# Kernel tuning notes

Measured on AMD Instinct MI355X. Metric: run time of the kernel, lower is better.

The kernel has to match this reference:

```python
import jax, jax.numpy as jnp
import numpy as np

NEG_SLOPE = 0.2  # PyG GATConv default LeakyReLU slope
EPS = 1e-16      # PyG softmax denominator epsilon


def _gat_layer(x, src, dst, W, a_src, a_dst, b, H, C):
    """One PyG-style GATConv layer (eval mode, add_self_loops already applied).
    x: [N, F_in], W: [F_in, H*C], a_src/a_dst: [H, C], b: [H*C]."""
    N = x.shape[0]
    h = (x @ W).reshape(N, H, C)                       # [N,H,C]
    alpha_src = jnp.sum(h * a_src, axis=-1)            # [N,H]
    alpha_dst = jnp.sum(h * a_dst, axis=-1)            # [N,H]
    e = jax.nn.leaky_relu(alpha_src[src] + alpha_dst[dst], NEG_SLOPE)  # [E,H]
    m = jax.ops.segment_max(e, dst, num_segments=N)    # [N,H] segment-softmax max
    p = jnp.exp(e - m[dst])                            # [E,H]
    s = jax.ops.segment_sum(p, dst, num_segments=N)    # [N,H]
    attn = p / (s[dst] + EPS)                          # [E,H]
    out = jax.ops.segment_sum(attn[:, :, None] * h[src], dst, num_segments=N)  # [N,H,C]
    return out.reshape(N, H * C) + b


def _add_self_loops(edge_index, N):
    loop = jnp.arange(N, dtype=edge_index.dtype)
    src = jnp.concatenate([edge_index[0], loop])
    dst = jnp.concatenate([edge_index[1], loop])
    return src, dst


def setup_inputs() -> dict:
    key = jax.random.key(0)
    N, E = 50000, 500000
    F_in, H, C = 336, 4, 128
    HC = H * C  # 512
    n_cls = 10
    ks = jax.random.split(key, 16)

    def glorot(k, shape):
        fan = shape[0] + shape[-1]
        return jax.random.normal(k, shape, jnp.float32) * jnp.sqrt(2.0 / fan)

    x = jax.random.normal(ks[0], (N, F_in), jnp.float32)
    edge_index = jax.random.randint(ks[1], (2, E), 0, N, dtype=jnp.int64)
    return {
        "x": x,
        "edge_index": edge_index,
        "W1": glorot(ks[2], (F_in, HC)),
        "a_src1": glorot(ks[3], (H, C)),
        "a_dst1": glorot(ks[4], (H, C)),
        "b1": jnp.zeros((HC,), jnp.float32),
        "W2": glorot(ks[5], (HC, HC)),
        "a_src2": glorot(ks[6], (H, C)),
        "a_dst2": glorot(ks[7], (H, C)),
        "b2": jnp.zeros((HC,), jnp.float32),
        "Wc1": glorot(ks[8], (HC, C)),
        "bc1": jnp.zeros((C,), jnp.float32),
        "Wc2": glorot(ks[9], (C, n_cls)),
        "bc2": jnp.zeros((n_cls,), jnp.float32),
    }


def reference(x, edge_index, W1, a_src1, a_dst1, b1, W2, a_src2, a_dst2, b2, Wc1, bc1, Wc2, bc2):
    H, C = 4, 128
    N = x.shape[0]
    src, dst = _add_self_loops(edge_index, N)
    h = _gat_layer(x, src, dst, W1, a_src1, a_dst1, b1, H, C)
    h = jax.nn.elu(h)  # ELU between layers only
    h = _gat_layer(h, src, dst, W2, a_src2, a_dst2, b2, H, C)
    # classifier (dropout is identity in eval)
    z = jax.nn.relu(h @ Wc1 + bc1)
    logits = z @ Wc2 + bc2
    return logits
```

## Files before the change

### kernel.cpp

```cpp
#include <hip/hip_runtime.h>
#include <math.h>

typedef unsigned short u16;
typedef unsigned int u32;
typedef short short8 __attribute__((ext_vector_type(8)));
typedef __bf16 bf16x8 __attribute__((ext_vector_type(8)));
typedef float f32x4 __attribute__((ext_vector_type(4)));
typedef u32 u32x4 __attribute__((ext_vector_type(4)));

typedef const __attribute__((address_space(1))) void* as1cv;
typedef __attribute__((address_space(3))) void* as3v;

__device__ __forceinline__ void gload16(const void* g, void* l) {
    __builtin_amdgcn_global_load_lds((as1cv)g, (as3v)l, 16, 0, 0);
}

__device__ __forceinline__ float b2f(u16 u) {
    union { u32 i; float f; } v; v.i = ((u32)u) << 16; return v.f;
}
__device__ __forceinline__ float b2f_lo(u32 q) {
    union { u32 i; float f; } v; v.i = q << 16; return v.f;
}
__device__ __forceinline__ float b2f_hi(u32 q) {
    union { u32 i; float f; } v; v.i = q & 0xffff0000u; return v.f;
}
__device__ __forceinline__ u16 f2b(float f) {
    union { float f; u32 i; } v; v.f = f;
    u32 i = v.i;
    u32 r = (i + 0x7fffu + ((i >> 16) & 1u)) >> 16;
    return (u16)r;
}
__device__ __forceinline__ u32 pack2(u16 a, u16 b) { return (u32)a | ((u32)b << 16); }


__device__ void agg_dev(const int* __restrict__ rowptr, const int* __restrict__ col,
                        const float* __restrict__ asrc, const float* __restrict__ adst,
                        const u16* __restrict__ hb, const float* __restrict__ bias,
                        u16* __restrict__ outb, int elu, int NODES) {
    const int wid = __builtin_amdgcn_readfirstlane((blockIdx.x * 256 + threadIdx.x) >> 6);
    const int nwaves = gridDim.x << 2;
    const int l = threadIdx.x & 63;
    const int hd = l >> 4;
    const int cbase = 8 * l;
    float bv[8];
#pragma unroll
    for (int c = 0; c < 8; c++) bv[c] = bias[cbase + c];

    for (int n = wid; n < NODES; n += nwaves) {
        const int beg = __builtin_amdgcn_readfirstlane(rowptr[n]);
        const int end = __builtin_amdgcn_readfirstlane(rowptr[n + 1]);
        const float ad = adst[n * 4 + hd];
        float acc0[8], acc1[8];
#pragma unroll
        for (int c = 0; c < 8; c++) { acc0[c] = 0.f; acc1[c] = 0.f; }
        float ss0 = 0.f, ss1 = 0.f;
        for (int j = beg; j < end; j += 8) {
            int s[8];
#pragma unroll
            for (int q = 0; q < 8; q++) {
                int jq = j + q;
                jq = jq < end ? jq : end - 1;
                s[q] = __builtin_amdgcn_readfirstlane(col[jq]);
            }
            u32x4 g[8];
#pragma unroll
            for (int q = 0; q < 8; q++)
                g[q] = *(const u32x4*)(hb + (size_t)s[q] * 512 + cbase);
            float p[8];
#pragma unroll
            for (int q = 0; q < 8; q++) {
                float e = asrc[(size_t)s[q] * 4 + hd] + ad;
                e = e > 0.f ? e : 0.2f * e;
                float pe = __expf(e);
                p[q] = (j + q < end) ? pe : 0.f;
            }
#pragma unroll
            for (int q = 0; q < 8; q += 2) {
                ss0 += p[q]; ss1 += p[q + 1];
#pragma unroll
                for (int u = 0; u < 4; u++) {
                    acc0[2 * u]     += p[q]     * b2f_lo(g[q][u]);
                    acc0[2 * u + 1] += p[q]     * b2f_hi(g[q][u]);
                    acc1[2 * u]     += p[q + 1] * b2f_lo(g[q + 1][u]);
                    acc1[2 * u + 1] += p[q + 1] * b2f_hi(g[q + 1][u]);
                }
            }
        }
        float inv = 1.f / (ss0 + ss1 + 1e-16f);
        float v[8];
#pragma unroll
        for (int c = 0; c < 8; c++) {
            float tv = (acc0[c] + acc1[c]) * inv + bv[c];
            if (elu) tv = tv > 0.f ? tv : expm1f(tv);
            v[c] = tv;
        }
        u32x4 ov;
        ov[0] = pack2(f2b(v[0]), f2b(v[1]));
        ov[1] = pack2(f2b(v[2]), f2b(v[3]));
        ov[2] = pack2(f2b(v[4]), f2b(v[5]));
        ov[3] = pack2(f2b(v[6]), f2b(v[7]));
        *(u32x4*)(outb + (size_t)n * 512 + cbase) = ov;
    }
}

__device__ void gemm_dev(const u16* __restrict__ A, const u16* __restrict__ Bt,
                         u16* __restrict__ C, const float* __restrict__ bias,
                         const float* __restrict__ aS, const float* __restrict__ aD,
                         float* __restrict__ asr, float* __restrict__ ads,
                         const float* __restrict__ Wc2, const float* __restrict__ bc2,
                         float* __restrict__ outp,
                         int M, int N, int K, int act, char* shm,
                         u16* As, u16* Bs, float (*red)[128][2]) {
    const int t = threadIdx.x;
    const int l = t & 63, w = t >> 6;

    const int nwg = gridDim.x * gridDim.y;
    const int fid = blockIdx.x + gridDim.x * blockIdx.y;
    int logical;
    {
        const int q = nwg >> 3, r = nwg & 7;
        const int xcd = fid & 7, ix = fid >> 3;
        logical = (xcd < r ? xcd * (q + 1) : r * (q + 1) + (xcd - r) * q) + ix;
    }
    const int gy = gridDim.y;
    const int mtile = logical / gy;
    const int hd_ = logical - mtile * gy;
    const int m0 = mtile * 128, n0 = hd_ * 128;

    const int wm = (w >> 1) * 64, wn = (w & 1) * 64;

    const int rl0 = w * 32 + (l >> 2);
    const int rl1 = rl0 + 16;
    const int gso = 8 * ((l & 3) ^ ((l >> 3) & 3));
    const u16* pA0 = A + (size_t)min(m0 + rl0, M - 1) * K + gso;
    const u16* pA1 = A + (size_t)min(m0 + rl1, M - 1) * K + gso;
    const u16* pB0 = Bt + (size_t)min(n0 + rl0, N - 1) * K + gso;
    const u16* pB1 = Bt + (size_t)min(n0 + rl1, N - 1) * K + gso;
    u16* lA0 = As + (size_t)(w * 32) * 32;
    u16* lA1 = lA0 + 16 * 32;
    u16* lB0 = Bs + (size_t)(w * 32) * 32;
    u16* lB1 = lB0 + 16 * 32;

    const int rs = ((l & 15) >> 1) & 3;
    const int roff = 8 * ((l >> 4) ^ rs);

    f32x4 acc[4][4];
    f32x4 z4 = {0.f, 0.f, 0.f, 0.f};
#pragma unroll
    for (int i = 0; i < 4; i++)
#pragma unroll
        for (int j = 0; j < 4; j++) acc[i][j] = z4;

    for (int k0 = 0; k0 < K; k0 += 32) {
        __syncthreads();
        gload16(pA0 + k0, lA0);
        gload16(pA1 + k0, lA1);
        gload16(pB0 + k0, lB0);
        gload16(pB1 + k0, lB1);
        __syncthreads();

        bf16x8 af[4], bfr[4];
#pragma unroll
        for (int i = 0; i < 4; i++) {
            af[i]  = *(const bf16x8*)(As + (wm + i * 16 + (l & 15)) * 32 + roff);
            bfr[i] = *(const bf16x8*)(Bs + (wn + i * 16 + (l & 15)) * 32 + roff);
        }
#pragma unroll
        for (int i = 0; i < 4; i++)
#pragma unroll
            for (int j = 0; j < 4; j++)
                acc[i][j] = __builtin_amdgcn_mfma_f32_16x16x32_bf16(af[i], bfr[j], acc[i][j], 0, 0, 0);
    }

    if (act == 2) {
        __syncthreads();
        float* wl = (float*)shm;
        float (*logbuf)[128][10] = (float (*)[128][10])(shm + 8192);
        for (int i = t; i < 1280; i += 256) wl[i] = Wc2[i];
        if (t < 10) wl[1280 + t] = bc2[t];
        __syncthreads();
        int cj[4];
#pragma unroll
        for (int j = 0; j < 4; j++) cj[j] = wn + j * 16 + (l & 15);
#pragma unroll
        for (int i = 0; i < 4; i++) {
#pragma unroll
            for (int r = 0; r < 4; r++) {
                float zv[4];
#pragma unroll
                for (int j = 0; j < 4; j++) {
                    float v = acc[i][j][r] + (bias ? bias[cj[j]] : 0.f);
                    zv[j] = v > 0.f ? v : 0.f;
                }
                float part[10];
#pragma unroll
                for (int k = 0; k < 10; k++) {
                    float s = 0.f;
#pragma unroll
                    for (int j = 0; j < 4; j++) s += zv[j] * wl[cj[j] * 10 + k];
#pragma unroll
                    for (int o = 1; o < 16; o <<= 1) s += __shfl_xor(s, o);
                    part[k] = s;
                }
                if ((l & 15) == 0) {
                    int rl = wm + i * 16 + (l >> 4) * 4 + r;
#pragma unroll
                    for (int k = 0; k < 10; k++) logbuf[w & 1][rl][k] = part[k];
                }
            }
        }
        __syncthreads();
        if (t < 128) {
            int row = m0 + t;
            if (row < M) {
#pragma unroll
                for (int k = 0; k < 10; k++)
                    outp[(size_t)row * 10 + k] =
                        logbuf[0][t][k] + logbuf[1][t][k] + wl[1280 + k];
            }
        }
        return;
    }

#pragma unroll
    for (int i = 0; i < 4; i++) {
        int rbase = m0 + wm + i * 16 + (l >> 4) * 4;
#pragma unroll
        for (int j = 0; j < 4; j++) {
            int c = n0 + wn + j * 16 + (l & 15);
            float bv = bias ? bias[c] : 0.f;
#pragma unroll
            for (int r = 0; r < 4; r++) {
                int row = rbase + r;
                if (row < M) {
                    float v = acc[i][j][r] + bv;
                    if (act == 1) v = v > 0.f ? v : 0.f;
                    C[(size_t)row * N + c] = f2b(v);
                }
            }
        }
    }

    if (aS) {
        const int hd = n0 >> 7;
        float aSv[4], aDv[4];
#pragma unroll
        for (int j = 0; j < 4; j++) {
            int c = n0 + wn + j * 16 + (l & 15);
            aSv[j] = aS[c];
            aDv[j] = aD[c];
        }
#pragma unroll
        for (int i = 0; i < 4; i++) {
#pragma unroll
            for (int r = 0; r < 4; r++) {
                float vs = 0.f, vd = 0.f;
#pragma unroll
                for (int j = 0; j < 4; j++) {
                    float hv = acc[i][j][r];
                    vs += hv * aSv[j];
                    vd += hv * aDv[j];
                }
#pragma unroll
                for (int o = 1; o < 16; o <<= 1) {
                    vs += __shfl_xor(vs, o);
                    vd += __shfl_xor(vd, o);
                }
                if ((l & 15) == 0) {
                    int rl = wm + i * 16 + (l >> 4) * 4 + r;
                    red[w & 1][rl][0] = vs;
                    red[w & 1][rl][1] = vd;
                }
            }
        }
        __syncthreads();
        if (t < 128) {
            int row = m0 + t;
            if (row < M) {
                asr[row * 4 + hd] = red[0][t][0] + red[1][t][0];
                ads[row * 4 + hd] = red[0][t][1] + red[1][t][1];
            }
        }
    }
}

__global__ __launch_bounds__(256) void BaselineGAT_41764261987077_kernel(
    int phase, int aux,
    const float* x, const int* ei,
    const float* W1, const float* as1, const float* ad1, const float* b1,
    const float* W2, const float* as2, const float* ad2, const float* b2,
    const float* Wc1, const float* bc1, const float* Wc2, const float* bc2,
    float* out,
    u16* hAb, u16* hbB, float* asr, float* ads,
    u16* xb, u16* w1t, u16* w2t, u16* wc1t,
    int* flag, int* cnt, int* tmp, int* bsum, int* boff,
    int* rowptr, int* cursor, int* col,
    const u16* gA, const u16* gB, u16* gC, const float* gBias,
    const float* gAs, const float* gAd,
    int gM, int gN, int gK, int gAct,
    int NODES, int E, int nblk)
{
    __shared__ f32x4 shm4[1156];
    char* shm = (char*)shm4;
    u16* As = (u16*)shm;
    u16* Bs = (u16*)(shm + 8192);
    float (*red)[128][2] = (float (*)[128][2])(shm + 16384);
    int* smi = (int*)shm;
    int* smb = (int*)(shm + 2048);

    const int t = threadIdx.x;
    const int gid = blockIdx.x * 256 + t;
    const int EN = E + NODES;

    switch (phase) {
    case 100: {
        if (gid < NODES * 10) out[gid] = 1000.0f;
    } break;
    case 0: {
        if (blockIdx.x == 0) {
            if (t == 0) smi[256] = 0;
            __syncthreads();
            for (int j = t; j < 1024; j += 256)
                if (ei[2 * j + 1] != 0) atomicAdd(&smi[256], 1);
            __syncthreads();
            if (t == 0) flag[0] = (smi[256] < 16) ? 2 : 1;
        } else {
            int i = (blockIdx.x - 1) * 256 + t;
            if (i < NODES) cnt[i] = 0;
        }
    } break;
    case 2: {
        if (gid >= EN) return;
        int step = flag[0];
        int d;
        if (gid < E) {
            d = ei[(size_t)(E + gid) * step];
            if ((unsigned)d >= (unsigned)NODES) d = 0;
        } else d = gid - E;
        atomicAdd(&cnt[d], 1);
    } break;
    case 3: {
        smi[t] = (gid < NODES) ? cnt[gid] : 0;
        __syncthreads();
        for (int o = 1; o < 256; o <<= 1) {
            int add = (t >= o) ? smi[t - o] : 0;
            __syncthreads();
            smi[t] += add;
            __syncthreads();
        }
        if (gid < NODES) tmp[gid] = smi[t];
        if (t == 255) bsum[blockIdx.x] = smi[255];
    } break;
    case 5: {
        smb[t] = (t < nblk) ? bsum[t] : 0;
        __syncthreads();
        for (int o = 1; o < 256; o <<= 1) {
            int add = (t >= o) ? smb[t - o] : 0;
            __syncthreads();
            smb[t] += add;
            __syncthreads();
        }
        int base = (blockIdx.x == 0) ? 0 : smb[blockIdx.x - 1];
        if (gid >= NODES) return;
        int incl = tmp[gid] + base;
        rowptr[gid + 1] = incl;
        cursor[gid] = incl - cnt[gid];
        if (gid == 0) rowptr[0] = 0;
    } break;
    case 6: {
        if (gid >= EN) return;
        int step = flag[0];
        int d, s;
        if (gid < E) {
            s = ei[(size_t)gid * step];
            d = ei[(size_t)(E + gid) * step];
            if ((unsigned)s >= (unsigned)NODES) s = 0;
            if ((unsigned)d >= (unsigned)NODES) d = 0;
        } else { d = gid - E; s = d; }
        int pos = atomicAdd(&cursor[d], 1);
        col[pos] = s;
    } break;
    case 20: {
        int i = gid;
        const int XC = NODES * 44;
        if (i < XC) {
            int n = i / 44, kk = (i - n * 44) * 8;
            short8 o;
            if (kk < 336) {
                const f32x4* xp = (const f32x4*)(x + (size_t)n * 336 + kk);
                f32x4 f0 = xp[0], f1 = xp[1];
                o[0] = (short)f2b(f0[0]); o[1] = (short)f2b(f0[1]);
                o[2] = (short)f2b(f0[2]); o[3] = (short)f2b(f0[3]);
                o[4] = (short)f2b(f1[0]); o[5] = (short)f2b(f1[1]);
                o[6] = (short)f2b(f1[2]); o[7] = (short)f2b(f1[3]);
            } else {
#pragma unroll
                for (int e = 0; e < 8; e++) o[e] = 0;
            }
            *(short8*)(xb + (size_t)n * 352 + kk) = o;
            return;
        }
        i -= XC;
        if (i < 512 * 352) {
            int n = i / 352, k = i - n * 352;
            w1t[i] = (k < 336) ? f2b(W1[(size_t)k * 512 + n]) : (u16)0;
            return;
        }
        i -= 512 * 352;
        if (i < 512 * 512) {
            int n = i >> 9, k = i & 511;
            w2t[i] = f2b(W2[(size_t)k * 512 + n]);
            return;
        }
        i -= 512 * 512;
        if (i < 128 * 512) {
            int n = i >> 9, k = i & 511;
            wc1t[i] = f2b(Wc1[(size_t)k * 128 + n]);
        }
    } break;
    case 30: gemm_dev(gA, gB, gC, gBias, gAs, gAd, asr, ads,
                      Wc2, bc2, out, gM, gN, gK, gAct, shm, As, Bs, red); break;
    case 31: agg_dev(rowptr, col, asr, ads, hAb, gBias, hbB, aux, NODES); break;
    }
}

extern "C" void kernel_launch(void* const* d_in, const int* in_sizes, int n_in,
                              void* d_out, int out_size, void* d_ws, size_t ws_size,
                              hipStream_t stream) {
    const float* x   = (const float*)d_in[0];
    const int*   ei  = (const int*)d_in[1];
    const float* W1  = (const float*)d_in[2];
    const float* as1 = (const float*)d_in[3];
    const float* ad1 = (const float*)d_in[4];
    const float* b1  = (const float*)d_in[5];
    const float* W2  = (const float*)d_in[6];
    const float* as2 = (const float*)d_in[7];
    const float* ad2 = (const float*)d_in[8];
    const float* b2  = (const float*)d_in[9];
    const float* Wc1 = (const float*)d_in[10];
    const float* bc1 = (const float*)d_in[11];
    const float* Wc2 = (const float*)d_in[12];
    const float* bc2 = (const float*)d_in[13];

    const int NODES = in_sizes[0] / 336;
    const int E     = in_sizes[1] / 2;

    char* ws = (char*)d_ws;
    size_t off = 0;
    auto alloc = [&](size_t b) -> char* {
        char* p = ws + off; off = (off + b + 255) & ~(size_t)255; return p;
    };
    u16*   xb   = (u16*)alloc((size_t)NODES * 352 * 2);
    u16*   hAb  = (u16*)alloc((size_t)NODES * 512 * 2);
    u16*   hbB  = (u16*)alloc((size_t)NODES * 512 * 2);
    float* asr  = (float*)alloc((size_t)NODES * 4 * 4);
    float* ads  = (float*)alloc((size_t)NODES * 4 * 4);
    u16*   w1t  = (u16*)alloc((size_t)512 * 352 * 2);
    u16*   w2t  = (u16*)alloc((size_t)512 * 512 * 2);
    u16*   wc1t = (u16*)alloc((size_t)128 * 512 * 2);
    int* flag   = (int*)alloc(256);
    int* cnt    = (int*)alloc((size_t)NODES * 4);
    int* tmp    = (int*)alloc((size_t)NODES * 4);
    int* bsum   = (int*)alloc(4096);
    int* boff   = (int*)alloc(4096);
    int* rowptr = (int*)alloc((size_t)(NODES + 1) * 4);
    int* cursor = (int*)alloc((size_t)NODES * 4);
    int* col    = (int*)alloc((size_t)(E + NODES) * 4);

    const int nblk = (NODES + 255) / 256;
    const int eblk = (E + NODES + 255) / 256;
    const int oblk = (out_size + 255) / 256;
    const int mt   = (NODES + 127) / 128;
    const int cvt_total = NODES * 44 + 512 * 352 + 512 * 512 + 128 * 512;

    auto L = [&](int phase, int aux, dim3 grid,
                 const u16* gA = nullptr, const u16* gB = nullptr,
                 u16* gC = nullptr, const float* gBias = nullptr,
                 const float* gAs = nullptr, const float* gAd = nullptr,
                 int gM = 0, int gN = 0, int gK = 0, int gAct = 0) {
        BaselineGAT_41764261987077_kernel<<<grid, 256, 0, stream>>>(
            phase, aux, x, ei, W1, as1, ad1, b1, W2, as2, ad2, b2,
            Wc1, bc1, Wc2, bc2, (float*)d_out,
            hAb, hbB, asr, ads, xb, w1t, w2t, wc1t,
            flag, cnt, tmp, bsum, boff, rowptr, cursor, col,
            gA, gB, gC, gBias, gAs, gAd, gM, gN, gK, gAct,
            NODES, E, nblk);
    };

    if (n_in < 14 || off > ws_size) { L(100, 1, oblk); return; }

    L(0, 0, nblk + 1);
    L(2, 0, eblk);
    L(3, 0, nblk);
    L(5, 0, nblk);
    L(6, 0, eblk);

    L(20, 0, (cvt_total + 255) / 256);

    L(30, 0, dim3(mt, 4), xb, w1t, hAb, nullptr, as1, ad1, NODES, 512, 352, 0);
    L(31, 1, 4096, nullptr, nullptr, nullptr, b1);

    L(30, 0, dim3(mt, 4), hbB, w2t, hAb, nullptr, as2, ad2, NODES, 512, 512, 0);
    L(31, 0, 4096, nullptr, nullptr, nullptr, b2);

    L(30, 0, dim3(mt, 1), hbB, wc1t, nullptr, bc1, nullptr, nullptr, NODES, 128, 512, 2);
}
```

Measured before the change: 593.0 us.

## Double-buffer GEMM LDS tiles to overlap global loads with MFMA

Splits the GEMM shared-memory tiles into two ping-pong buffers so the next K-slice is fetched via global_load_lds while the current slice runs MFMAs. This cuts one barrier per iteration and hides load latency. It also raises wave priority around the MFMA block. Shared memory roughly doubles, which may reduce occupancy, and the extra barrier before the act==2 epilogue is dropped because the loop already ends with one.

Result: faster. 576.5 us (-2.8%).

```diff
diff --git a/kernel.cpp b/kernel.cpp
--- a/kernel.cpp
+++ b/kernel.cpp
@@ -110,7 +110,8 @@
                          const float* __restrict__ Wc2, const float* __restrict__ bc2,
                          float* __restrict__ outp,
                          int M, int N, int K, int act, char* shm,
-                         u16* As, u16* Bs, float (*red)[128][2]) {
+                         u16* As0, u16* As1, u16* Bs0, u16* Bs1,
+                         float (*red)[128][2]) {
     const int t = threadIdx.x;
     const int l = t & 63, w = t >> 6;
 
@@ -136,10 +137,7 @@
     const u16* pA1 = A + (size_t)min(m0 + rl1, M - 1) * K + gso;
     const u16* pB0 = Bt + (size_t)min(n0 + rl0, N - 1) * K + gso;
     const u16* pB1 = Bt + (size_t)min(n0 + rl1, N - 1) * K + gso;
-    u16* lA0 = As + (size_t)(w * 32) * 32;
-    u16* lA1 = lA0 + 16 * 32;
-    u16* lB0 = Bs + (size_t)(w * 32) * 32;
-    u16* lB1 = lB0 + 16 * 32;
+    const int wbase = (w * 32) * 32;
 
     const int rs = ((l & 15) >> 1) & 3;
     const int roff = 8 * ((l >> 4) ^ rs);
@@ -151,29 +149,44 @@
 #pragma unroll
         for (int j = 0; j < 4; j++) acc[i][j] = z4;
 
-    for (int k0 = 0; k0 < K; k0 += 32) {
-        __syncthreads();
-        gload16(pA0 + k0, lA0);
-        gload16(pA1 + k0, lA1);
-        gload16(pB0 + k0, lB0);
-        gload16(pB1 + k0, lB1);
-        __syncthreads();
-
+    auto STAGE = [&](u16* As_, u16* Bs_, int k0) {
+        gload16(pA0 + k0, As_ + wbase);
+        gload16(pA1 + k0, As_ + wbase + 16 * 32);
+        gload16(pB0 + k0, Bs_ + wbase);
+        gload16(pB1 + k0, Bs_ + wbase + 16 * 32);
+    };
+    auto COMP = [&](const u16* As_, const u16* Bs_) {
         bf16x8 af[4], bfr[4];
 #pragma unroll
         for (int i = 0; i < 4; i++) {
-            af[i]  = *(const bf16x8*)(As + (wm + i * 16 + (l & 15)) * 32 + roff);
-            bfr[i] = *(const bf16x8*)(Bs + (wn + i * 16 + (l & 15)) * 32 + roff);
-        }
+            af[i]  = *(const bf16x8*)(As_ + (wm + i * 16 + (l & 15)) * 32 + roff);
+            bfr[i] = *(const bf16x8*)(Bs_ + (wn + i * 16 + (l & 15)) * 32 + roff);
+        }
+        __builtin_amdgcn_s_setprio(1);
 #pragma unroll
         for (int i = 0; i < 4; i++)
 #pragma unroll
             for (int j = 0; j < 4; j++)
                 acc[i][j] = __builtin_amdgcn_mfma_f32_16x16x32_bf16(af[i], bfr[j], acc[i][j], 0, 0, 0);
+        __builtin_amdgcn_s_setprio(0);
+    };
+
+    const int ns = K >> 5;
+    STAGE(As0, Bs0, 0);
+    __syncthreads();
+    int s = 0;
+    while (true) {
+        if (s + 1 < ns) STAGE(As1, Bs1, (s + 1) << 5);
+        COMP(As0, Bs0);
+        __syncthreads();
+        if (++s >= ns) break;
+        if (s + 1 < ns) STAGE(As0, Bs0, (s + 1) << 5);
+        COMP(As1, Bs1);
+        __syncthreads();
+        if (++s >= ns) break;
     }
 
     if (act == 2) {
-        __syncthreads();
         float* wl = (float*)shm;
         float (*logbuf)[128][10] = (float (*)[128][10])(shm + 8192);
         for (int i = t; i < 1280; i += 256) wl[i] = Wc2[i];
@@ -195,12 +208,12 @@
                 float part[10];
 #pragma unroll
                 for (int k = 0; k < 10; k++) {
-                    float s = 0.f;
-#pragma unroll
-                    for (int j = 0; j < 4; j++) s += zv[j] * wl[cj[j] * 10 + k];
-#pragma unroll
-                    for (int o = 1; o < 16; o <<= 1) s += __shfl_xor(s, o);
-                    part[k] = s;
+                    float s2 = 0.f;
+#pragma unroll
+                    for (int j = 0; j < 4; j++) s2 += zv[j] * wl[cj[j] * 10 + k];
+#pragma unroll
+                    for (int o = 1; o < 16; o <<= 1) s2 += __shfl_xor(s2, o);
+                    part[k] = s2;
                 }
                 if ((l & 15) == 0) {
                     int rl = wm + i * 16 + (l >> 4) * 4 + r;
@@ -300,11 +313,13 @@
     int gM, int gN, int gK, int gAct,
     int NODES, int E, int nblk)
 {
-    __shared__ f32x4 shm4[1156];
+    __shared__ f32x4 shm4[2176];
     char* shm = (char*)shm4;
-    u16* As = (u16*)shm;
-    u16* Bs = (u16*)(shm + 8192);
-    float (*red)[128][2] = (float (*)[128][2])(shm + 16384);
+    u16* As0 = (u16*)shm;
+    u16* As1 = (u16*)(shm + 8192);
+    u16* Bs0 = (u16*)(shm + 16384);
+    u16* Bs1 = (u16*)(shm + 24576);
+    float (*red)[128][2] = (float (*)[128][2])(shm + 32768);
     int* smi = (int*)shm;
     int* smb = (int*)(shm + 2048);
 
@@ -419,7 +434,8 @@
         }
     } break;
     case 30: gemm_dev(gA, gB, gC, gBias, gAs, gAd, asr, ads,
-                      Wc2, bc2, out, gM, gN, gK, gAct, shm, As, Bs, red); break;
+                      Wc2, bc2, out, gM, gN, gK, gAct, shm,
+                      As0, As1, Bs0, Bs1, red); break;
     case 31: agg_dev(rowptr, col, asr, ads, hAb, gBias, hbB, aux, NODES); break;
     }
 }
```
